# Kernel tuning notes

Hardware: AMD Instinct MI355X
Metric: run time of the kernel (lower is better)

Reference implementation:

```python
import jax, jax.numpy as jnp
import numpy as np

B, T, C, H = 4, 2048, 1024, 16
D = C // H  # head_dim = 64
ROPE_BASE = 10000.0
EPS = 1e-6


def _rms_norm(x):
    return x / jnp.sqrt(jnp.mean(x * x, axis=-1, keepdims=True) + EPS)


def _rope_tables(t_len, d, dtype):
    inv_freq = 1.0 / (ROPE_BASE ** (jnp.arange(0, d, 2, dtype=jnp.float32) / d))
    t = jnp.arange(t_len, dtype=jnp.float32)
    freqs = jnp.outer(t, inv_freq)  # [T, D/2]
    return jnp.cos(freqs).astype(dtype)[None, None], jnp.sin(freqs).astype(dtype)[None, None]


def _apply_rotary(x, cos, sin):
    d = x.shape[-1] // 2
    x1, x2 = x[..., :d], x[..., d:]
    return jnp.concatenate([x1 * cos + x2 * sin, -x1 * sin + x2 * cos], axis=-1)


def setup_inputs() -> dict:
    key = jax.random.key(0)
    k1, k2, k3, k4, k5 = jax.random.split(key, 5)
    x = jax.random.normal(k1, (B, T, C), dtype=jnp.float32)
    Wqkv = jax.random.normal(k2, (C, 3 * C), dtype=jnp.float32) * 0.02
    bqkv = jax.random.normal(k3, (3 * C,), dtype=jnp.float32) * 0.02
    # NOTE: original zero-inits c_proj.weight; randomized here for a non-trivial baseline.
    Wproj = jax.random.normal(k4, (C, C), dtype=jnp.float32) * 0.02
    bproj = jax.random.normal(k5, (C,), dtype=jnp.float32) * 0.02
    lamb = jnp.float32(0.5)
    return {"x": x, "Wqkv": Wqkv, "bqkv": bqkv, "Wproj": Wproj, "bproj": bproj, "lamb": lamb}


def reference(x, Wqkv, bqkv, Wproj, bproj, lamb):
    b, t, c = x.shape
    qkv = x @ Wqkv + bqkv  # [B,T,3C]
    q, k, v = jnp.split(qkv, 3, axis=-1)
    # [B,T,C] -> [B,H,T,D]
    to_heads = lambda z: z.reshape(b, t, H, D).transpose(0, 2, 1, 3)
    query, key_, value = to_heads(q), to_heads(k), to_heads(v)
    # v1 defaults to value -> blend is identity, kept for faithfulness
    value = (1.0 - lamb) * value + lamb * value
    query = _rms_norm(query)
    key_ = _rms_norm(key_)
    cos, sin = _rope_tables(t, D, x.dtype)
    query = _apply_rotary(query, cos, sin)
    key_ = _apply_rotary(key_, cos, sin)
    # causal SDPA
    scale = 1.0 / jnp.sqrt(jnp.float32(D)).astype(x.dtype)
    scores = jnp.einsum('bhqd,bhkd->bhqk', query, key_) * scale
    causal = jnp.tril(jnp.ones((t, t), dtype=bool))
    scores = jnp.where(causal[None, None], scores, jnp.finfo(scores.dtype).min)
    probs = jax.nn.softmax(scores, axis=-1)
    attn = jnp.einsum('bhqk,bhkd->bhqd', probs, value)
    attn = attn.transpose(0, 2, 1, 3).reshape(b, t, c)
    out = attn @ Wproj + bproj
    return out, value
```

## Files before the change

kernel.cpp:

```cpp
#include <hip/hip_runtime.h>
#include <math.h>

#define B_   4
#define T_   2048
#define C_   1024
#define H_   16
#define D_   64
#define TC3  3072

typedef __attribute__((ext_vector_type(8))) short short8;
typedef __attribute__((ext_vector_type(4))) short short4b;
typedef __attribute__((ext_vector_type(8))) unsigned short ushortv8;
typedef __attribute__((ext_vector_type(4))) float f32x4;
typedef __attribute__((ext_vector_type(4))) __bf16 bf16x4;

__device__ __forceinline__ float bf2f(unsigned short u) {
  unsigned int x = ((unsigned int)u) << 16;
  float f; __builtin_memcpy(&f, &x, 4); return f;
}
__device__ __forceinline__ unsigned short f2bf(float f) {
  unsigned int x; __builtin_memcpy(&x, &f, 4);
  x += 0x7fff + ((x >> 16) & 1);
  return (unsigned short)(x >> 16);
}

#define MFMA32(a, b, c) __builtin_amdgcn_mfma_f32_16x16x32_bf16(a, b, c, 0, 0, 0)
#if __has_builtin(__builtin_amdgcn_mfma_f32_16x16x16_bf16)
#define MFMA16(a, b, c) __builtin_amdgcn_mfma_f32_16x16x16_bf16(a, b, c, 0, 0, 0)
#else
#define MFMA16(a, b, c) __builtin_amdgcn_mfma_f32_16x16x16bf16_1k(a, b, c, 0, 0, 0)
#endif

#define GLOAD_LDS(gp, lp) __builtin_amdgcn_global_load_lds( \
    (const __attribute__((address_space(1))) unsigned int*)(gp), \
    (__attribute__((address_space(3))) unsigned int*)(lp), 16, 0, 0)

__global__ __launch_bounds__(256)
void convert_bf16(const float* __restrict__ x, unsigned short* __restrict__ xb) {
  const size_t i = ((size_t)blockIdx.x * 256 + threadIdx.x) * 8;
  float4 f0 = *(const float4*)(x + i);
  float4 f1 = *(const float4*)(x + i + 4);
  ushortv8 u = { f2bf(f0.x), f2bf(f0.y), f2bf(f0.z), f2bf(f0.w),
                 f2bf(f1.x), f2bf(f1.y), f2bf(f1.z), f2bf(f1.w) };
  *(ushortv8*)(xb + i) = u;
}

__global__ __launch_bounds__(256)
void transpose_bf16(const float* __restrict__ W, unsigned short* __restrict__ WT,
                    int K, int N) {
  __shared__ float tile[64][65];
  const int k0 = blockIdx.y * 64, n0 = blockIdx.x * 64;
  const int r = threadIdx.x >> 4, c4 = (threadIdx.x & 15) * 4;
#pragma unroll
  for (int p = 0; p < 4; ++p) {
    int kk = p * 16 + r;
    float4 v = *(const float4*)(W + (size_t)(k0 + kk) * N + n0 + c4);
    tile[kk][c4 + 0] = v.x; tile[kk][c4 + 1] = v.y;
    tile[kk][c4 + 2] = v.z; tile[kk][c4 + 3] = v.w;
  }
  __syncthreads();
#pragma unroll
  for (int p = 0; p < 4; ++p) {
    int nn = p * 16 + r;
    ushort4 o = { f2bf(tile[c4 + 0][nn]), f2bf(tile[c4 + 1][nn]),
                  f2bf(tile[c4 + 2][nn]), f2bf(tile[c4 + 3][nn]) };
    *(ushort4*)(WT + (size_t)(n0 + nn) * K + k0 + c4) = o;
  }
}

template<bool OUT_BF16>
__global__ __launch_bounds__(256)
void gemm_mfma(const unsigned short* __restrict__ Ab,
               const unsigned short* __restrict__ Bt,
               const float* __restrict__ bias, void* __restrict__ Cv,
               int K, int lda, int ldb, int ldc) {
  __shared__ unsigned short As[128 * 64];
  __shared__ unsigned short Bs[128 * 64];
  const int tid = threadIdx.x;
  const int l = tid & 63, w = tid >> 6;
  const int m0 = blockIdx.y * 128, n0 = blockIdx.x * 128;
  const int wm = (w & 1) * 64, wn = (w >> 1) * 64;
  const int fr = l & 15, g = l >> 4;

  f32x4 acc[4][4];
#pragma unroll
  for (int i = 0; i < 4; ++i)
#pragma unroll
    for (int j = 0; j < 4; ++j) acc[i][j] = (f32x4)0.f;

  const int gr = l >> 3;
  const int gc = (l & 7) ^ gr;

  for (int kt = 0; kt < K; kt += 64) {
    __syncthreads();
#pragma unroll
    for (int q = 0; q < 4; ++q) {
      int rr = (w * 4 + q) * 8 + gr;
      GLOAD_LDS(Ab + (size_t)(m0 + rr) * lda + kt + gc * 8,
                &As[(w * 4 + q) * 512]);
      GLOAD_LDS(Bt + (size_t)(n0 + rr) * ldb + kt + gc * 8,
                &Bs[(w * 4 + q) * 512]);
    }
    __syncthreads();

#pragma unroll
    for (int s = 0; s < 2; ++s) {
      const int cofs = (((s * 4 + g) ^ (fr & 7)) << 3);
      short8 a[4], b[4];
#pragma unroll
      for (int i = 0; i < 4; ++i)
        a[i] = *(const short8*)&As[(wm + i * 16 + fr) * 64 + cofs];
#pragma unroll
      for (int j = 0; j < 4; ++j)
        b[j] = *(const short8*)&Bs[(wn + j * 16 + fr) * 64 + cofs];
#pragma unroll
      for (int i = 0; i < 4; ++i)
#pragma unroll
        for (int j = 0; j < 4; ++j)
          acc[i][j] = MFMA32(a[i], b[j], acc[i][j]);
    }
  }

#pragma unroll
  for (int j = 0; j < 4; ++j) {
    const int n = n0 + wn + j * 16 + fr;
    const float bv = bias[n];
#pragma unroll
    for (int i = 0; i < 4; ++i) {
#pragma unroll
      for (int rg = 0; rg < 4; ++rg) {
        const int m = m0 + wm + i * 16 + g * 4 + rg;
        float v = acc[i][j][rg] + bv;
        if (OUT_BF16) ((unsigned short*)Cv)[(size_t)m * ldc + n] = f2bf(v);
        else          ((float*)Cv)[(size_t)m * ldc + n] = v;
      }
    }
  }
}

__global__ __launch_bounds__(256)
void rmsrope_kernel(unsigned short* __restrict__ qkv) {
  const int unit = blockIdx.x * 4 + (threadIdx.x >> 6);
  const int lane = threadIdx.x & 63;
  const int b = unit / (T_ * H_);
  const int rem = unit % (T_ * H_);
  const int t = rem / H_;
  const int h = rem % H_;
  const size_t base = (size_t)(b * T_ + t) * TC3;

  const int i = lane & 31;
  const float inv = __builtin_amdgcn_exp2f(-13.2877123795494f * (float)(2 * i)
                                           * (1.0f / 64.0f));
  const float ang = (float)t * inv;
  const float cs = cosf(ang);
  const float sn = sinf(ang);

  {
    const size_t idx = base + h * 64 + lane;
    float q = bf2f(qkv[idx]);
    float ss = q * q;
    ss += __shfl_xor(ss, 32); ss += __shfl_xor(ss, 16);
    ss += __shfl_xor(ss, 8);  ss += __shfl_xor(ss, 4);
    ss += __shfl_xor(ss, 2);  ss += __shfl_xor(ss, 1);
    float qn = q * (1.0f / sqrtf(ss * (1.0f / 64.0f) + 1e-6f));
    float part = __shfl_xor(qn, 32);
    float out = (lane < 32) ? (qn * cs + part * sn) : (qn * cs - part * sn);
    qkv[idx] = f2bf(out);
  }
  {
    const size_t idx = base + C_ + h * 64 + lane;
    float k = bf2f(qkv[idx]);
    float ss = k * k;
    ss += __shfl_xor(ss, 32); ss += __shfl_xor(ss, 16);
    ss += __shfl_xor(ss, 8);  ss += __shfl_xor(ss, 4);
    ss += __shfl_xor(ss, 2);  ss += __shfl_xor(ss, 1);
    float kn = k * (1.0f / sqrtf(ss * (1.0f / 64.0f) + 1e-6f));
    float part = __shfl_xor(kn, 32);
    float out = (lane < 32) ? (kn * cs + part * sn) : (kn * cs - part * sn);
    qkv[idx] = f2bf(out);
  }
}

__global__ __launch_bounds__(256)
void vtrans_kernel(const unsigned short* __restrict__ qkv,
                   const float* __restrict__ lambp,
                   unsigned short* __restrict__ vT,
                   float* __restrict__ valOut) {
  __shared__ float tile[64][65];
  const int t0 = blockIdx.x * 64;
  const int head = blockIdx.y;
  const int b = head >> 4, h = head & 15;
  const float lamb = lambp[0];
  const int r = threadIdx.x >> 4, c4 = (threadIdx.x & 15) * 4;
#pragma unroll
  for (int p = 0; p < 4; ++p) {
    int tt = p * 16 + r;
    ushort4 raw = *(const ushort4*)(
        qkv + (size_t)(b * T_ + t0 + tt) * TC3 + 2 * C_ + h * 64 + c4);
    float4 f;
    f.x = (1.f - lamb) * bf2f(raw.x) + lamb * bf2f(raw.x);
    f.y = (1.f - lamb) * bf2f(raw.y) + lamb * bf2f(raw.y);
    f.z = (1.f - lamb) * bf2f(raw.z) + lamb * bf2f(raw.z);
    f.w = (1.f - lamb) * bf2f(raw.w) + lamb * bf2f(raw.w);
    tile[tt][c4 + 0] = f.x; tile[tt][c4 + 1] = f.y;
    tile[tt][c4 + 2] = f.z; tile[tt][c4 + 3] = f.w;
    *(float4*)(valOut + ((size_t)head * T_ + t0 + tt) * D_ + c4) = f;
  }
  __syncthreads();
#pragma unroll
  for (int p = 0; p < 4; ++p) {
    int d = p * 16 + r;
    ushort4 o = { f2bf(tile[c4 + 0][d]), f2bf(tile[c4 + 1][d]),
                  f2bf(tile[c4 + 2][d]), f2bf(tile[c4 + 3][d]) };
    *(ushort4*)(vT + ((size_t)head * D_ + d) * T_ + t0 + c4) = o;
  }
}

#define SCL_ (0.125f * 1.44269504088896f)

__device__ __forceinline__ void attn_tile(
    const unsigned short* Ks,
    const unsigned short* Vs,
    const short8 (&qf)[2][2], int qrow0 , int k0,
    int fr, int quad, int f8,
    float (&l_pt)[2], f32x4 (&o)[2][4]) {
  f32x4 st[2][4];
#pragma unroll
  for (int i = 0; i < 2; ++i)
#pragma unroll
    for (int j = 0; j < 4; ++j) st[i][j] = (f32x4)0.f;

  __builtin_amdgcn_s_setprio(1);
#pragma unroll
  for (int kc = 0; kc < 2; ++kc) {
    const int cofs = (((kc * 4 + quad) ^ f8) << 3);
#pragma unroll
    for (int j = 0; j < 4; ++j) {
      short8 kf = *(const short8*)&Ks[(j * 16 + fr) * 64 + cofs];
      st[0][j] = MFMA32(kf, qf[kc][0], st[0][j]);
      st[1][j] = MFMA32(kf, qf[kc][1], st[1][j]);
    }
  }
  __builtin_amdgcn_s_setprio(0);

  short4b pa[2][4];
#pragma unroll
  for (int i = 0; i < 2; ++i) {
    const int qg = qrow0 + i * 16 + fr;
#pragma unroll
    for (int j = 0; j < 4; ++j) {
      const int kg = k0 + j * 16 + quad * 4;
#pragma unroll
      for (int r = 0; r < 4; ++r) {
        float arg = st[i][j][r] * SCL_;
        if (kg + r > qg) arg = -INFINITY;
        float p = __builtin_amdgcn_exp2f(arg);
        l_pt[i] += p;
        st[i][j][r] = p;
      }
      bf16x4 pb = { (__bf16)st[i][j][0], (__bf16)st[i][j][1],
                    (__bf16)st[i][j][2], (__bf16)st[i][j][3] };
      pa[i][j] = __builtin_bit_cast(short4b, pb);
    }
  }

  __builtin_amdgcn_s_setprio(1);
#pragma unroll
  for (int c = 0; c < 4; ++c) {
    const int vofs = ((((c * 2 + (quad >> 1)) ^ f8) << 3) + (quad & 1) * 4);
#pragma unroll
    for (int jd = 0; jd < 4; ++jd) {
      short4b vf = *(const short4b*)&Vs[(jd * 16 + fr) * 64 + vofs];
      o[0][jd] = MFMA16(pa[0][c], vf, o[0][jd]);
      o[1][jd] = MFMA16(pa[1][c], vf, o[1][jd]);
    }
  }
  __builtin_amdgcn_s_setprio(0);
}

__device__ __forceinline__ void attn_store(
    unsigned short* __restrict__ qkv, int bT, int h, int qrow0,
    int fr, int quad, float (&l_pt)[2], f32x4 (&o)[2][4]) {
#pragma unroll
  for (int i = 0; i < 2; ++i) {
    float lv = l_pt[i];
    lv += __shfl_xor(lv, 16);
    lv += __shfl_xor(lv, 32);
    float inv = 1.0f / lv;
    float invq[4];
#pragma unroll
    for (int r = 0; r < 4; ++r) invq[r] = __shfl(inv, quad * 4 + r);
#pragma unroll
    for (int jd = 0; jd < 4; ++jd) {
      const int d = jd * 16 + fr;
#pragma unroll
      for (int r = 0; r < 4; ++r) {
        const int row = qrow0 + i * 16 + quad * 4 + r;
        qkv[(size_t)(bT + row) * TC3 + 2 * C_ + h * 64 + d] =
            f2bf(o[i][jd][r] * invq[r]);
      }
    }
  }
}

__global__ __launch_bounds__(256)
void flash_mfma(unsigned short* __restrict__ qkv,
                const unsigned short* __restrict__ vT) {
  __shared__ unsigned short KV[2][2][64 * 64];

  const int z = blockIdx.z;
  const int xx = ((int)blockIdx.x + ((z >> 1) << 3)) & 15;
  const int qt = (z & 1) ? (15 - xx) : xx;
  const int b  = z;
  const int h  = blockIdx.y;
  const int bT = b * T_;

  const int tid = threadIdx.x;
  const int w = tid >> 6, l = tid & 63;
  const int fr = l & 15, quad = l >> 4;
  const int q0 = qt * 128;
  const int gr = l >> 3;
  const int gc = (l & 7) ^ gr;
  const int f8 = fr & 7;

#define STAGE(KS, VS, KT) do { \
  const int _k0 = (KT) * 64; \
  _Pragma("unroll") \
  for (int s_ = 0; s_ < 2; ++s_) { \
    int row_ = w * 16 + s_ * 8; \
    GLOAD_LDS(qkv + (size_t)(bT + _k0 + row_ + gr) * TC3 + C_ + h * 64 + gc * 8, \
              &(KS)[row_ * 64]); \
    GLOAD_LDS(vT + ((size_t)(b * H_ + h) * D_ + row_ + gr) * T_ + _k0 + gc * 8, \
              &(VS)[row_ * 64]); \
  } \
} while (0)

  unsigned short* Qb = &KV[0][0][0];
#pragma unroll
  for (int s = 0; s < 4; ++s) {
    int rbase = w * 32 + s * 8;
    GLOAD_LDS(qkv + (size_t)(bT + q0 + rbase + gr) * TC3 + h * 64 + gc * 8,
              Qb + rbase * 64);
  }
  STAGE(KV[1][0], KV[1][1], 0);
  __syncthreads();

  short8 qf[2][2];
#pragma unroll
  for (int kc = 0; kc < 2; ++kc) {
    const int cofs = (((kc * 4 + quad) ^ f8) << 3);
    qf[kc][0] = *(const short8*)&Qb[(w * 32 + fr) * 64 + cofs];
    qf[kc][1] = *(const short8*)&Qb[(w * 32 + 16 + fr) * 64 + cofs];
  }
  __syncthreads();

  float l_pt[2] = {0.f, 0.f};
  f32x4 o[2][4];
#pragma unroll
  for (int i = 0; i < 2; ++i)
#pragma unroll
    for (int j = 0; j < 4; ++j) o[i][j] = (f32x4)0.f;

  const int nk = 2 * qt + 2;
  const int qr0 = q0 + w * 32;

  int cur = 1;
  for (int kt = 0; kt < nk; ++kt) {
    const int nxt = cur ^ 1;
    if (kt + 1 < nk) {
      STAGE(KV[nxt][0], KV[nxt][1], kt + 1);
      asm volatile("s_waitcnt vmcnt(4)" ::: "memory");
    } else {
      asm volatile("s_waitcnt vmcnt(0)" ::: "memory");
    }
    __builtin_amdgcn_s_barrier();
    asm volatile("" ::: "memory");

    attn_tile(&KV[cur][0][0], &KV[cur][1][0], qf, qr0, kt * 64,
              fr, quad, f8, l_pt, o);

    if (kt + 1 < nk) {
      __builtin_amdgcn_s_barrier();
      asm volatile("" ::: "memory");
    }
    cur = nxt;
  }

  attn_store(qkv, bT, h, qr0, fr, quad, l_pt, o);
#undef STAGE
}

extern "C" void kernel_launch(void* const* d_in, const int* in_sizes, int n_in,
                              void* d_out, int out_size, void* d_ws, size_t ws_size,
                              hipStream_t stream) {
  const float* x     = (const float*)d_in[0];
  const float* Wqkv  = (const float*)d_in[1];
  const float* bqkv  = (const float*)d_in[2];
  const float* Wproj = (const float*)d_in[3];
  const float* bproj = (const float*)d_in[4];
  const float* lamb  = (const float*)d_in[5];

  float* out     = (float*)d_out;
  float* val_out = out + (size_t)B_ * T_ * C_;

  unsigned short* qkvb   = (unsigned short*)d_ws;
  unsigned short* WqkvT  = qkvb + (size_t)B_ * T_ * TC3;
  unsigned short* WprojT = WqkvT + (size_t)TC3 * C_;
  unsigned short* vT     = WprojT + (size_t)C_ * C_;
  unsigned short* xb     = vT + (size_t)B_ * H_ * D_ * T_;

  convert_bf16<<<dim3((B_ * T_ * C_) / 2048), 256, 0, stream>>>(x, xb);
  transpose_bf16<<<dim3(TC3 / 64, C_ / 64), 256, 0, stream>>>(Wqkv, WqkvT, C_, TC3);
  transpose_bf16<<<dim3(C_ / 64, C_ / 64), 256, 0, stream>>>(Wproj, WprojT, C_, C_);

  gemm_mfma<true><<<dim3(TC3 / 128, (B_ * T_) / 128), 256, 0, stream>>>(
      xb, WqkvT, bqkv, qkvb, C_, C_, C_, TC3);

  rmsrope_kernel<<<dim3((B_ * T_ * H_) / 4), 256, 0, stream>>>(qkvb);

  vtrans_kernel<<<dim3(T_ / 64, B_ * H_), 256, 0, stream>>>(qkvb, lamb, vT, val_out);

  flash_mfma<<<dim3(16, H_, B_), 256, 0, stream>>>(qkvb, vT);

  gemm_mfma<false><<<dim3(C_ / 128, (B_ * T_) / 128), 256, 0, stream>>>(
      qkvb + 2 * C_, WprojT, bproj, out, C_, TC3, C_, C_);
}
```

Measured before the change: 326.5 us.

## Halve flash attention query tile to 64 rows and fold softmax scale into RoPE

The attention kernel now gives each block 64 query rows instead of 128, with one 16-row MFMA group per wave. The grid doubles to 32 query tiles, which raises block count and evens out the causal load across CUs. The softmax scale times log2(e) is folded into the query RoPE coefficients, so the per-element multiply in the softmax loop goes away. In exchange, each K/V tile loaded into LDS is reused by half as many query rows, so global-to-LDS traffic per unit of compute doubles. The scaled query is also rounded to bf16 after scaling, which slightly changes numerics.

```diff
diff --git a/kernel.cpp b/kernel.cpp
--- a/kernel.cpp
+++ b/kernel.cpp
@@ -34,6 +34,8 @@
 #define GLOAD_LDS(gp, lp) __builtin_amdgcn_global_load_lds( \
     (const __attribute__((address_space(1))) unsigned int*)(gp), \
     (__attribute__((address_space(3))) unsigned int*)(lp), 16, 0, 0)
+
+#define QSCL (0.125f * 1.44269504088896f)
 
 __global__ __launch_bounds__(256)
 void convert_bf16(const float* __restrict__ x, unsigned short* __restrict__ xb) {
@@ -154,6 +156,7 @@
   const float ang = (float)t * inv;
   const float cs = cosf(ang);
   const float sn = sinf(ang);
+  const float csq = cs * QSCL, snq = sn * QSCL;
 
   {
     const size_t idx = base + h * 64 + lane;
@@ -164,7 +167,7 @@
     ss += __shfl_xor(ss, 2);  ss += __shfl_xor(ss, 1);
     float qn = q * (1.0f / sqrtf(ss * (1.0f / 64.0f) + 1e-6f));
     float part = __shfl_xor(qn, 32);
-    float out = (lane < 32) ? (qn * cs + part * sn) : (qn * cs - part * sn);
+    float out = (lane < 32) ? (qn * csq + part * snq) : (qn * csq - part * snq);
     qkv[idx] = f2bf(out);
   }
   {
@@ -216,19 +219,16 @@
   }
 }
 
-#define SCL_ (0.125f * 1.44269504088896f)
 
 __device__ __forceinline__ void attn_tile(
     const unsigned short* Ks,
     const unsigned short* Vs,
-    const short8 (&qf)[2][2], int qrow0 , int k0,
+    const short8 (&qf)[2], int qrow0 , int k0,
     int fr, int quad, int f8,
-    float (&l_pt)[2], f32x4 (&o)[2][4]) {
-  f32x4 st[2][4];
-#pragma unroll
-  for (int i = 0; i < 2; ++i)
-#pragma unroll
-    for (int j = 0; j < 4; ++j) st[i][j] = (f32x4)0.f;
+    float &l_pt, f32x4 (&o)[4]) {
+  f32x4 st[4];
+#pragma unroll
+  for (int j = 0; j < 4; ++j) st[j] = (f32x4)0.f;
 
   __builtin_amdgcn_s_setprio(1);
 #pragma unroll
@@ -237,31 +237,27 @@
 #pragma unroll
     for (int j = 0; j < 4; ++j) {
       short8 kf = *(const short8*)&Ks[(j * 16 + fr) * 64 + cofs];
-      st[0][j] = MFMA32(kf, qf[kc][0], st[0][j]);
-      st[1][j] = MFMA32(kf, qf[kc][1], st[1][j]);
+      st[j] = MFMA32(kf, qf[kc], st[j]);
     }
   }
   __builtin_amdgcn_s_setprio(0);
 
-  short4b pa[2][4];
-#pragma unroll
-  for (int i = 0; i < 2; ++i) {
-    const int qg = qrow0 + i * 16 + fr;
-#pragma unroll
-    for (int j = 0; j < 4; ++j) {
-      const int kg = k0 + j * 16 + quad * 4;
-#pragma unroll
-      for (int r = 0; r < 4; ++r) {
-        float arg = st[i][j][r] * SCL_;
-        if (kg + r > qg) arg = -INFINITY;
-        float p = __builtin_amdgcn_exp2f(arg);
-        l_pt[i] += p;
-        st[i][j][r] = p;
-      }
-      bf16x4 pb = { (__bf16)st[i][j][0], (__bf16)st[i][j][1],
-                    (__bf16)st[i][j][2], (__bf16)st[i][j][3] };
-      pa[i][j] = __builtin_bit_cast(short4b, pb);
-    }
+  short4b pa[4];
+  const int qg = qrow0 + fr;
+#pragma unroll
+  for (int j = 0; j < 4; ++j) {
+    const int kg = k0 + j * 16 + quad * 4;
+#pragma unroll
+    for (int r = 0; r < 4; ++r) {
+      float arg = st[j][r];
+      if (kg + r > qg) arg = -INFINITY;
+      float p = __builtin_amdgcn_exp2f(arg);
+      l_pt += p;
+      st[j][r] = p;
+    }
+    bf16x4 pb = { (__bf16)st[j][0], (__bf16)st[j][1],
+                  (__bf16)st[j][2], (__bf16)st[j][3] };
+    pa[j] = __builtin_bit_cast(short4b, pb);
   }
 
   __builtin_amdgcn_s_setprio(1);
@@ -271,36 +267,10 @@
 #pragma unroll
     for (int jd = 0; jd < 4; ++jd) {
       short4b vf = *(const short4b*)&Vs[(jd * 16 + fr) * 64 + vofs];
-      o[0][jd] = MFMA16(pa[0][c], vf, o[0][jd]);
-      o[1][jd] = MFMA16(pa[1][c], vf, o[1][jd]);
+      o[jd] = MFMA16(pa[c], vf, o[jd]);
     }
   }
   __builtin_amdgcn_s_setprio(0);
-}
-
-__device__ __forceinline__ void attn_store(
-    unsigned short* __restrict__ qkv, int bT, int h, int qrow0,
-    int fr, int quad, float (&l_pt)[2], f32x4 (&o)[2][4]) {
-#pragma unroll
-  for (int i = 0; i < 2; ++i) {
-    float lv = l_pt[i];
-    lv += __shfl_xor(lv, 16);
-    lv += __shfl_xor(lv, 32);
-    float inv = 1.0f / lv;
-    float invq[4];
-#pragma unroll
-    for (int r = 0; r < 4; ++r) invq[r] = __shfl(inv, quad * 4 + r);
-#pragma unroll
-    for (int jd = 0; jd < 4; ++jd) {
-      const int d = jd * 16 + fr;
-#pragma unroll
-      for (int r = 0; r < 4; ++r) {
-        const int row = qrow0 + i * 16 + quad * 4 + r;
-        qkv[(size_t)(bT + row) * TC3 + 2 * C_ + h * 64 + d] =
-            f2bf(o[i][jd][r] * invq[r]);
-      }
-    }
-  }
 }
 
 __global__ __launch_bounds__(256)
@@ -309,8 +279,8 @@
   __shared__ unsigned short KV[2][2][64 * 64];
 
   const int z = blockIdx.z;
-  const int xx = ((int)blockIdx.x + ((z >> 1) << 3)) & 15;
-  const int qt = (z & 1) ? (15 - xx) : xx;
+  const int xx = ((int)blockIdx.x + ((z >> 1) << 3)) & 31;
+  const int qt = (z & 1) ? (31 - xx) : xx;
   const int b  = z;
   const int h  = blockIdx.y;
   const int bT = b * T_;
@@ -318,7 +288,7 @@
   const int tid = threadIdx.x;
   const int w = tid >> 6, l = tid & 63;
   const int fr = l & 15, quad = l >> 4;
-  const int q0 = qt * 128;
+  const int q0 = qt * 64;
   const int gr = l >> 3;
   const int gc = (l & 7) ^ gr;
   const int f8 = fr & 7;
@@ -336,33 +306,31 @@
 } while (0)
 
   unsigned short* Qb = &KV[0][0][0];
-#pragma unroll
-  for (int s = 0; s < 4; ++s) {
-    int rbase = w * 32 + s * 8;
+  {
+    int rbase = w * 16;
     GLOAD_LDS(qkv + (size_t)(bT + q0 + rbase + gr) * TC3 + h * 64 + gc * 8,
               Qb + rbase * 64);
+    GLOAD_LDS(qkv + (size_t)(bT + q0 + rbase + 8 + gr) * TC3 + h * 64 + gc * 8,
+              Qb + (rbase + 8) * 64);
   }
   STAGE(KV[1][0], KV[1][1], 0);
   __syncthreads();
 
-  short8 qf[2][2];
+  short8 qf[2];
 #pragma unroll
   for (int kc = 0; kc < 2; ++kc) {
     const int cofs = (((kc * 4 + quad) ^ f8) << 3);
-    qf[kc][0] = *(const short8*)&Qb[(w * 32 + fr) * 64 + cofs];
-    qf[kc][1] = *(const short8*)&Qb[(w * 32 + 16 + fr) * 64 + cofs];
+    qf[kc] = *(const short8*)&Qb[(w * 16 + fr) * 64 + cofs];
   }
   __syncthreads();
 
-  float l_pt[2] = {0.f, 0.f};
-  f32x4 o[2][4];
-#pragma unroll
-  for (int i = 0; i < 2; ++i)
-#pragma unroll
-    for (int j = 0; j < 4; ++j) o[i][j] = (f32x4)0.f;
-
-  const int nk = 2 * qt + 2;
-  const int qr0 = q0 + w * 32;
+  float l_pt = 0.f;
+  f32x4 o[4];
+#pragma unroll
+  for (int j = 0; j < 4; ++j) o[j] = (f32x4)0.f;
+
+  const int nk = qt + 1;
+  const int qr0 = q0 + w * 16;
 
   int cur = 1;
   for (int kt = 0; kt < nk; ++kt) {
@@ -386,7 +354,25 @@
     cur = nxt;
   }
 
-  attn_store(qkv, bT, h, qr0, fr, quad, l_pt, o);
+  {
+    float lv = l_pt;
+    lv += __shfl_xor(lv, 16);
+    lv += __shfl_xor(lv, 32);
+    float inv = 1.0f / lv;
+    float invq[4];
+#pragma unroll
+    for (int r = 0; r < 4; ++r) invq[r] = __shfl(inv, quad * 4 + r);
+#pragma unroll
+    for (int jd = 0; jd < 4; ++jd) {
+      const int d = jd * 16 + fr;
+#pragma unroll
+      for (int r = 0; r < 4; ++r) {
+        const int row = qr0 + quad * 4 + r;
+        qkv[(size_t)(bT + row) * TC3 + 2 * C_ + h * 64 + d] =
+            f2bf(o[jd][r] * invq[r]);
+      }
+    }
+  }
 #undef STAGE
 }
 
@@ -420,7 +406,7 @@
 
   vtrans_kernel<<<dim3(T_ / 64, B_ * H_), 256, 0, stream>>>(qkvb, lamb, vT, val_out);
 
-  flash_mfma<<<dim3(16, H_, B_), 256, 0, stream>>>(qkvb, vT);
+  flash_mfma<<<dim3(32, H_, B_), 256, 0, stream>>>(qkvb, vT);
 
   gemm_mfma<false><<<dim3(C_ / 128, (B_ * T_) / 128), 256, 0, stream>>>(
       qkvb + 2 * C_, WprojT, bproj, out, C_, TC3, C_, C_);
```

New measurement: 327.5 us. Within noise of the previous version (+0.3%).

## Fuse RMS norm, RoPE and softmax scale into QKV GEMM epilogue

Applied to the files above, without the earlier changes.

Moves the per-head RMS normalisation and rotary embedding into the QKV GEMM epilogue, reducing across the 64-column warp tile with lane shuffles, and drops the separate rmsrope kernel. This removes one launch plus a full read and write of Q and K in bf16. The softmax scale and log2(e) are folded into Q before rounding, so attention skips one multiply per score. The costs are extra epilogue registers and transcendental work in the GEMM, fast __sinf/__cosf at angles up to 2047 that may lose accuracy, and Q rounded to bf16 after scaling.

```diff
diff --git a/kernel.cpp b/kernel.cpp
--- a/kernel.cpp
+++ b/kernel.cpp
@@ -34,6 +34,8 @@
 #define GLOAD_LDS(gp, lp) __builtin_amdgcn_global_load_lds( \
     (const __attribute__((address_space(1))) unsigned int*)(gp), \
     (__attribute__((address_space(3))) unsigned int*)(lp), 16, 0, 0)
+
+#define QSCL (0.125f * 1.44269504088896f)
 
 __global__ __launch_bounds__(256)
 void convert_bf16(const float* __restrict__ x, unsigned short* __restrict__ xb) {
@@ -68,7 +70,7 @@
   }
 }
 
-template<bool OUT_BF16>
+template<bool OUT_BF16, bool FUSE_RMSROPE>
 __global__ __launch_bounds__(256)
 void gemm_mfma(const unsigned short* __restrict__ Ab,
                const unsigned short* __restrict__ Bt,
@@ -121,6 +123,62 @@
     }
   }
 
+  if (FUSE_RMSROPE && n0 < 2 * C_) {
+    const float qscl = (n0 < C_) ? QSCL : 1.0f;
+    float bvj[4];
+#pragma unroll
+    for (int j = 0; j < 4; ++j) bvj[j] = bias[n0 + wn + j * 16 + fr];
+#pragma unroll
+    for (int i = 0; i < 4; ++i)
+#pragma unroll
+      for (int j = 0; j < 4; ++j)
+#pragma unroll
+        for (int rg = 0; rg < 4; ++rg) acc[i][j][rg] += bvj[j];
+
+    float invf[2];
+#pragma unroll
+    for (int jp = 0; jp < 2; ++jp)
+      invf[jp] = __builtin_amdgcn_exp2f(-13.2877123795494f *
+                                        (float)(2 * (jp * 16 + fr)) *
+                                        (1.0f / 64.0f));
+#pragma unroll
+    for (int i = 0; i < 4; ++i) {
+#pragma unroll
+      for (int rg = 0; rg < 4; ++rg) {
+        float ss = 0.f;
+#pragma unroll
+        for (int j = 0; j < 4; ++j) ss += acc[i][j][rg] * acc[i][j][rg];
+        ss += __shfl_xor(ss, 1); ss += __shfl_xor(ss, 2);
+        ss += __shfl_xor(ss, 4); ss += __shfl_xor(ss, 8);
+        const float s = 1.0f / sqrtf(ss * (1.0f / 64.0f) + 1e-6f);
+        const int m = m0 + wm + i * 16 + g * 4 + rg;
+        const float t = (float)(m & (T_ - 1));
+#pragma unroll
+        for (int jp = 0; jp < 2; ++jp) {
+          float x1 = acc[i][jp][rg] * s;
+          float x2 = acc[i][jp + 2][rg] * s;
+          float ang = t * invf[jp];
+          float cs = __cosf(ang) * qscl;
+          float sn = __sinf(ang) * qscl;
+          acc[i][jp][rg]     = x1 * cs + x2 * sn;
+          acc[i][jp + 2][rg] = x2 * cs - x1 * sn;
+        }
+      }
+    }
+#pragma unroll
+    for (int j = 0; j < 4; ++j) {
+      const int n = n0 + wn + j * 16 + fr;
+#pragma unroll
+      for (int i = 0; i < 4; ++i)
+#pragma unroll
+        for (int rg = 0; rg < 4; ++rg) {
+          const int m = m0 + wm + i * 16 + g * 4 + rg;
+          ((unsigned short*)Cv)[(size_t)m * ldc + n] = f2bf(acc[i][j][rg]);
+        }
+    }
+    return;
+  }
+
 #pragma unroll
   for (int j = 0; j < 4; ++j) {
     const int n = n0 + wn + j * 16 + fr;
@@ -135,49 +193,6 @@
         else          ((float*)Cv)[(size_t)m * ldc + n] = v;
       }
     }
-  }
-}
-
-__global__ __launch_bounds__(256)
-void rmsrope_kernel(unsigned short* __restrict__ qkv) {
-  const int unit = blockIdx.x * 4 + (threadIdx.x >> 6);
-  const int lane = threadIdx.x & 63;
-  const int b = unit / (T_ * H_);
-  const int rem = unit % (T_ * H_);
-  const int t = rem / H_;
-  const int h = rem % H_;
-  const size_t base = (size_t)(b * T_ + t) * TC3;
-
-  const int i = lane & 31;
-  const float inv = __builtin_amdgcn_exp2f(-13.2877123795494f * (float)(2 * i)
-                                           * (1.0f / 64.0f));
-  const float ang = (float)t * inv;
-  const float cs = cosf(ang);
-  const float sn = sinf(ang);
-
-  {
-    const size_t idx = base + h * 64 + lane;
-    float q = bf2f(qkv[idx]);
-    float ss = q * q;
-    ss += __shfl_xor(ss, 32); ss += __shfl_xor(ss, 16);
-    ss += __shfl_xor(ss, 8);  ss += __shfl_xor(ss, 4);
-    ss += __shfl_xor(ss, 2);  ss += __shfl_xor(ss, 1);
-    float qn = q * (1.0f / sqrtf(ss * (1.0f / 64.0f) + 1e-6f));
-    float part = __shfl_xor(qn, 32);
-    float out = (lane < 32) ? (qn * cs + part * sn) : (qn * cs - part * sn);
-    qkv[idx] = f2bf(out);
-  }
-  {
-    const size_t idx = base + C_ + h * 64 + lane;
-    float k = bf2f(qkv[idx]);
-    float ss = k * k;
-    ss += __shfl_xor(ss, 32); ss += __shfl_xor(ss, 16);
-    ss += __shfl_xor(ss, 8);  ss += __shfl_xor(ss, 4);
-    ss += __shfl_xor(ss, 2);  ss += __shfl_xor(ss, 1);
-    float kn = k * (1.0f / sqrtf(ss * (1.0f / 64.0f) + 1e-6f));
-    float part = __shfl_xor(kn, 32);
-    float out = (lane < 32) ? (kn * cs + part * sn) : (kn * cs - part * sn);
-    qkv[idx] = f2bf(out);
   }
 }
 
@@ -216,7 +231,6 @@
   }
 }
 
-#define SCL_ (0.125f * 1.44269504088896f)
 
 __device__ __forceinline__ void attn_tile(
     const unsigned short* Ks,
@@ -252,7 +266,7 @@
       const int kg = k0 + j * 16 + quad * 4;
 #pragma unroll
       for (int r = 0; r < 4; ++r) {
-        float arg = st[i][j][r] * SCL_;
+        float arg = st[i][j][r];
         if (kg + r > qg) arg = -INFINITY;
         float p = __builtin_amdgcn_exp2f(arg);
         l_pt[i] += p;
@@ -413,15 +427,13 @@
   transpose_bf16<<<dim3(TC3 / 64, C_ / 64), 256, 0, stream>>>(Wqkv, WqkvT, C_, TC3);
   transpose_bf16<<<dim3(C_ / 64, C_ / 64), 256, 0, stream>>>(Wproj, WprojT, C_, C_);
 
-  gemm_mfma<true><<<dim3(TC3 / 128, (B_ * T_) / 128), 256, 0, stream>>>(
+  gemm_mfma<true, true><<<dim3(TC3 / 128, (B_ * T_) / 128), 256, 0, stream>>>(
       xb, WqkvT, bqkv, qkvb, C_, C_, C_, TC3);
 
-  rmsrope_kernel<<<dim3((B_ * T_ * H_) / 4), 256, 0, stream>>>(qkvb);
-
   vtrans_kernel<<<dim3(T_ / 64, B_ * H_), 256, 0, stream>>>(qkvb, lamb, vT, val_out);
 
   flash_mfma<<<dim3(16, H_, B_), 256, 0, stream>>>(qkvb, vT);
 
-  gemm_mfma<false><<<dim3(C_ / 128, (B_ * T_) / 128), 256, 0, stream>>>(
+  gemm_mfma<false, false><<<dim3(C_ / 128, (B_ * T_) / 128), 256, 0, stream>>>(
       qkvb + 2 * C_, WprojT, bproj, out, C_, TC3, C_, C_);
 }
```

Result: faster. 318.7 us (-2.4%).
